# Performance work log

Measured on AMD Instinct MI355X. Metric: run time of the kernel, lower is better.

The kernel has to match this reference:

```python
import jax, jax.numpy as jnp
import numpy as np

N_NODES = 100000
IN_CH = 256
H1, C1 = 8, 8   # conv1: heads=8, out_channels=8
H2, C2 = 1, 3   # conv2: heads=1, out_channels=3
NEG_SLOPE = 0.2
EPS = 1e-16


def gat_conv(x, src, dst, W, a_src, a_dst, b, heads, out_ch, n_nodes):
    """PyG-style GATConv (eval mode, self-loops already in src/dst)."""
    h = (x @ W).reshape(n_nodes, heads, out_ch)          # [N,H,C]
    alpha_s = jnp.einsum('nhc,hc->nh', h, a_src)         # [N,H]
    alpha_d = jnp.einsum('nhc,hc->nh', h, a_dst)         # [N,H]
    e = alpha_s[src] + alpha_d[dst]                      # [E,H]
    e = jnp.where(e > 0, e, NEG_SLOPE * e)               # leaky_relu(0.2)
    # segment softmax over destination nodes
    m = jax.ops.segment_max(e, dst, num_segments=n_nodes)
    m = jnp.where(jnp.isfinite(m), m, 0.0)
    ex = jnp.exp(e - m[dst])
    s = jax.ops.segment_sum(ex, dst, num_segments=n_nodes)
    a = ex / (s[dst] + EPS)                              # [E,H]
    msg = h[src] * a[:, :, None]                         # [E,H,C]
    out = jax.ops.segment_sum(msg, dst, num_segments=n_nodes)  # [N,H,C]
    return out.reshape(n_nodes, heads * out_ch) + b


def setup_inputs() -> dict:
    key = jax.random.key(0)
    ks = jax.random.split(key, 10)
    x = jax.random.normal(ks[0], (N_NODES, IN_CH), dtype=jnp.float32)
    edge_index = jax.random.randint(ks[1], (2, 3200000), 0, N_NODES, dtype=jnp.int64)
    sc = 0.1
    return {
        'x': x,
        'edge_index': edge_index,
        'W1': jax.random.normal(ks[2], (IN_CH, H1 * C1), dtype=jnp.float32) * sc,
        'a_src1': jax.random.normal(ks[3], (H1, C1), dtype=jnp.float32) * sc,
        'a_dst1': jax.random.normal(ks[4], (H1, C1), dtype=jnp.float32) * sc,
        'b1': jnp.zeros((H1 * C1,), dtype=jnp.float32),
        'W2': jax.random.normal(ks[5], (H1 * C1, H2 * C2), dtype=jnp.float32) * sc,
        'a_src2': jax.random.normal(ks[6], (H2, C2), dtype=jnp.float32) * sc,
        'a_dst2': jax.random.normal(ks[7], (H2, C2), dtype=jnp.float32) * sc,
        'b2': jnp.zeros((H2 * C2,), dtype=jnp.float32),
    }


def reference(x, edge_index, W1, a_src1, a_dst1, b1, W2, a_src2, a_dst2, b2):
    n = x.shape[0]
    loop = jnp.arange(n, dtype=edge_index.dtype)
    src = jnp.concatenate([edge_index[0], loop])  # add_self_loops=True
    dst = jnp.concatenate([edge_index[1], loop])
    h = gat_conv(x, src, dst, W1, a_src1, a_dst1, b1, H1, C1, n)
    h = jax.nn.elu(h)
    out = gat_conv(h, src, dst, W2, a_src2, a_dst2, b2, H2, C2, n)
    return out
```

## Files before the change

kernel.cpp:

```cpp
#include <hip/hip_runtime.h>
#include <hip/hip_bf16.h>

#define P_W1  0
#define P_AS1 16384
#define P_AD1 16448
#define P_B1  16512
#define P_W2  16576
#define P_AS2 16768
#define P_AD2 16771
#define P_B2  16774

#define NBLK_CSR 512
#define G1GRID   1024

typedef __attribute__((ext_vector_type(8))) short short8;
typedef __attribute__((ext_vector_type(8))) unsigned short ushort8v;
typedef __attribute__((ext_vector_type(4))) float floatx4;

__device__ __forceinline__ float ldf(const void* p, int i, int bf) {
  if (bf) {
    unsigned v = ((unsigned)((const unsigned short*)p)[i]) << 16;
    float f; __builtin_memcpy(&f, &v, 4); return f;
  }
  return ((const float*)p)[i];
}
__device__ __forceinline__ int ldi(const void* p, long i, int i64) {
  return i64 ? ((const int*)p)[2*i] : ((const int*)p)[i];
}
__device__ __forceinline__ unsigned short f2bfbits(float f) {
  __hip_bfloat16 b = __float2bfloat16(f);
  unsigned short u; __builtin_memcpy(&u, &b, 2); return u;
}
__device__ __forceinline__ float bf2f(unsigned short u) {
  unsigned v = ((unsigned)u) << 16;
  float f; __builtin_memcpy(&f, &v, 4); return f;
}

__device__ __forceinline__ void bar_lgkm() {
  __builtin_amdgcn_sched_barrier(0);
  asm volatile("s_waitcnt lgkmcnt(0)" ::: "memory");
  __builtin_amdgcn_s_barrier();
  __builtin_amdgcn_sched_barrier(0);
}

__global__ void k_prep(const void* x, const void* ei,
                       const void* w1, const void* as1, const void* ad1, const void* b1,
                       const void* w2, const void* as2, const void* ad2, const void* b2,
                       int* flags, float* params, unsigned short* w1t) {
  __shared__ int sh[2];
  int tid = threadIdx.x, lane = tid & 63, w = tid >> 6;
  if (w == 0) {
    const unsigned* xw = (const unsigned*)x;
    int hits = 0;
    for (int i = lane; i < 256; i += 64) {
      unsigned b = (xw[i] >> 7) & 0xFF;
      hits += (b >= 96 && b <= 141) ? 1 : 0;
    }
    for (int o = 32; o >= 1; o >>= 1) hits += __shfl_xor(hits, o);
    if (lane == 0) sh[0] = (hits >= 160) ? 1 : 0;
  } else if (w == 1) {
    const unsigned* ew = (const unsigned*)ei;
    int z = 0;
    for (int i = lane; i < 128; i += 64) z += (ew[2*i+1] == 0u) ? 1 : 0;
    for (int o = 32; o >= 1; o >>= 1) z += __shfl_xor(z, o);
    if (lane == 0) sh[1] = (z >= 64) ? 1 : 0;
  }
  __syncthreads();
  int bf = sh[0];
  if (tid == 0) { flags[0] = sh[0]; flags[1] = sh[1]; }
  for (int i = tid; i < 16384; i += blockDim.x) {
    int ch = i >> 8, k = i & 255;
    w1t[i] = f2bfbits(ldf(w1, k * 64 + ch, bf));
  }
  if (!bf) {
    for (int i = tid; i < 16384; i += blockDim.x) params[P_W1 + i] = ldf(w1, i, bf);
  }
  for (int i = tid; i < 64; i += blockDim.x) {
    params[P_AS1 + i] = ldf(as1, i, bf);
    params[P_AD1 + i] = ldf(ad1, i, bf);
    params[P_B1  + i] = ldf(b1,  i, bf);
  }
  for (int i = tid; i < 192; i += blockDim.x) params[P_W2 + i] = ldf(w2, i, bf);
  for (int i = tid; i < 3; i += blockDim.x) {
    params[P_AS2 + i] = ldf(as2, i, bf);
    params[P_AD2 + i] = ldf(ad2, i, bf);
    params[P_B2  + i] = ldf(b2,  i, bf);
  }
}

__global__ void k_bcount(const void* ei, const int* flags, int* gcnt, int* brsv,
                         int E0, int N, int NB, int chunk) {
  __shared__ int h[256];
  int tid = threadIdx.x;
  int i64 = flags[1];
  for (int j = tid; j < NB; j += 256) h[j] = 0;
  __syncthreads();
  int E = E0 + N;
  int b0 = blockIdx.x * chunk, b1 = min(b0 + chunk, E);
  const int* ep = (const int*)ei;
  for (int e = b0 + tid * 2; e < b1; e += 512) {
    int d0, d1;
    if (e + 1 < E0) {
      if (i64) { int4 v = *(const int4*)(ep + 2 * ((long)E0 + e)); d0 = v.x; d1 = v.z; }
      else     { int2 v = *(const int2*)(ep + (long)E0 + e);       d0 = v.x; d1 = v.y; }
    } else {
      d0 = (e < E0)     ? ldi(ei, (long)E0 + e, i64)     : (e - E0);
      d1 = (e + 1 < E0) ? ldi(ei, (long)E0 + e + 1, i64) : (e + 1 - E0);
    }
    atomicAdd(&h[d0 >> 9], 1);
    if (e + 1 < b1) atomicAdd(&h[d1 >> 9], 1);
  }
  __syncthreads();
  for (int j = tid; j < NB; j += 256)
    brsv[blockIdx.x * NB + j] = atomicAdd(&gcnt[j], h[j]);
}

__global__ void k_bbase(const int* gcnt, int* bbase, int NB) {
  __shared__ int sh[256];
  int tid = threadIdx.x;
  sh[tid] = (tid < NB) ? gcnt[tid] : 0;
  __syncthreads();
  int own = sh[tid];
  for (int ofs = 1; ofs < 256; ofs <<= 1) {
    int v = (tid >= ofs) ? sh[tid - ofs] : 0;
    __syncthreads();
    sh[tid] += v;
    __syncthreads();
  }
  if (tid < NB) bbase[tid] = sh[tid] - own;
  if (tid == NB - 1) bbase[NB] = sh[tid];
}

__global__ void k_bscatter(const void* ei, const int* flags, const int* bbase,
                           const int* brsv, unsigned* pairs, int E0, int N, int NB, int chunk) {
  __shared__ int base_s[256];
  __shared__ int rnk[256];
  int i64 = flags[1], tid = threadIdx.x;
  for (int j = tid; j < NB; j += 256) {
    base_s[j] = bbase[j] + brsv[blockIdx.x * NB + j];
    rnk[j] = 0;
  }
  __syncthreads();
  int E = E0 + N;
  int b0 = blockIdx.x * chunk, b1 = min(b0 + chunk, E);
  const int* ep = (const int*)ei;
  for (int e = b0 + tid * 2; e < b1; e += 512) {
    int s0v, s1v, d0, d1;
    if (e + 1 < E0) {
      if (i64) {
        int4 vs = *(const int4*)(ep + 2 * (long)e);        s0v = vs.x; s1v = vs.z;
        int4 vd = *(const int4*)(ep + 2 * ((long)E0 + e)); d0 = vd.x;  d1 = vd.z;
      } else {
        int2 vs = *(const int2*)(ep + (long)e);            s0v = vs.x; s1v = vs.y;
        int2 vd = *(const int2*)(ep + (long)E0 + e);       d0 = vd.x;  d1 = vd.y;
      }
    } else {
      if (e < E0) { s0v = ldi(ei, e, i64);     d0 = ldi(ei, (long)E0 + e, i64); }
      else        { s0v = e - E0;              d0 = s0v; }
      if (e + 1 < E0) { s1v = ldi(ei, e + 1, i64); d1 = ldi(ei, (long)E0 + e + 1, i64); }
      else            { s1v = e + 1 - E0;          d1 = s1v; }
    }
    {
      int bkt = d0 >> 9;
      int r = atomicAdd(&rnk[bkt], 1);
      pairs[base_s[bkt] + r] = ((unsigned)s0v << 9) | (unsigned)(d0 & 511);
    }
    if (e + 1 < b1) {
      int bkt = d1 >> 9;
      int r = atomicAdd(&rnk[bkt], 1);
      pairs[base_s[bkt] + r] = ((unsigned)s1v << 9) | (unsigned)(d1 & 511);
    }
  }
}

__global__ void k_bsort(const unsigned* pairs, const int* bbase, int* rowp,
                        int* srcs, int N, int NB, int E) {
  __shared__ int h0[512], sc[512], rk[512];
  int b = blockIdx.x, tid = threadIdx.x;
  int s0 = bbase[b], s1 = bbase[b + 1], L = s1 - s0;
  for (int j = tid; j < 512; j += 256) { h0[j] = 0; rk[j] = 0; }
  __syncthreads();
  for (int i = tid; i < L; i += 256) atomicAdd(&h0[pairs[s0 + i] & 511], 1);
  __syncthreads();
  for (int j = tid; j < 512; j += 256) sc[j] = h0[j];
  __syncthreads();
  for (int ofs = 1; ofs < 512; ofs <<= 1) {
    int j0 = tid, j1 = tid + 256;
    int v0 = (j0 >= ofs) ? sc[j0 - ofs] : 0;
    int v1 = (j1 >= ofs) ? sc[j1 - ofs] : 0;
    __syncthreads();
    sc[j0] += v0; sc[j1] += v1;
    __syncthreads();
  }
  for (int j = tid; j < 512; j += 256) {
    int off = sc[j] - h0[j];
    int node = (b << 9) + j;
    if (node < N) rowp[node] = s0 + off;
    sc[j] = off;
  }
  if (b == 0 && tid == 0) rowp[N] = E;
  __syncthreads();
  for (int i = tid; i < L; i += 256) {
    unsigned p = pairs[s0 + i];
    int j = p & 511;
    int r = atomicAdd(&rk[j], 1);
    srcs[s0 + sc[j] + r] = (int)(p >> 9);
  }
}

__device__ __forceinline__ void gemm1_f32(const float* x, const float* params,
                                          unsigned short* h1, float* a_s, float* a_d,
                                          int N, int wave, int lane) {
  int n0 = wave * 4;
  if (n0 >= N) return;
  int nb[4];
#pragma unroll
  for (int j = 0; j < 4; j++) nb[j] = min(n0 + j, N - 1) * 256;
  float acc[4] = {0.f, 0.f, 0.f, 0.f};
  const float* W = params + P_W1;
  for (int k = 0; k < 256; k++) {
    float wv = W[k * 64 + lane];
#pragma unroll
    for (int j = 0; j < 4; j++) acc[j] += x[nb[j] + k] * wv;
  }
  float as1v = params[P_AS1 + lane], ad1v = params[P_AD1 + lane];
#pragma unroll
  for (int j = 0; j < 4; j++) {
    int n = n0 + j;
    if (n >= N) break;
    float hv = acc[j];
    float s = hv * as1v, d = hv * ad1v;
    s += __shfl_xor(s, 1); s += __shfl_xor(s, 2); s += __shfl_xor(s, 4);
    d += __shfl_xor(d, 1); d += __shfl_xor(d, 2); d += __shfl_xor(d, 4);
    h1[(size_t)n * 64 + lane] = f2bfbits(hv);
    if ((lane & 7) == 0) {
      a_s[n * 8 + (lane >> 3)] = s;
      a_d[n * 8 + (lane >> 3)] = d;
    }
  }
}

__global__ void k_gemm1(const void* x, const unsigned short* w1t, const int* flags,
                        const float* params, unsigned short* h1, float* a_s, float* a_d, int N) {
  __shared__ __align__(16) char smem[32768];
  int tid = threadIdx.x;
  int w = tid >> 6, lane = tid & 63;
  if (flags[0]) {
    int NT = (N + 31) >> 5;
    int l16 = lane & 15, quad = lane >> 4;
    int ch = w * 16 + l16;
    const char* xb = (const char*)x;

    auto stage = [&](int t, int bsel) {
      int row0 = t << 5;
      char* buf = smem + bsel * 16384;
#pragma unroll
      for (int jj = 0; jj < 4; jj++) {
        int g = w * 256 + jj * 64 + lane;
        int r = g >> 5;
        int c = g & 31;
        int gr = row0 + r; if (gr >= N) gr = N - 1;
        const char* src = xb + (size_t)gr * 512 + (size_t)((c << 4) ^ ((r & 7) << 4));
        char* dst = buf + g * 16;
        __builtin_amdgcn_global_load_lds((const __attribute__((address_space(1))) unsigned int*)src,
                                         (__attribute__((address_space(3))) unsigned int*)dst,
                                         16, 0, 0);
      }
    };

    short8 bfr[8];
    const unsigned short* wp = w1t + (size_t)ch * 256 + quad * 8;
#pragma unroll
    for (int i = 0; i < 8; i++) bfr[i] = *(const short8*)(wp + i * 32);
    __builtin_amdgcn_sched_barrier(0);

    int t0 = blockIdx.x;
    if (t0 < NT) stage(t0, 0);
    int cur = 0;
    for (int t = t0; t < NT; t += G1GRID) {
      __syncthreads();
      if (t + G1GRID < NT) stage(t + G1GRID, cur ^ 1);
      int row0 = t << 5;
      const char* buf = smem + cur * 16384;
      floatx4 acc[2];
#pragma unroll
      for (int rg = 0; rg < 2; rg++) {
        floatx4 a4 = {0.f, 0.f, 0.f, 0.f};
        int r = rg * 16 + l16;
        const char* arow = buf + r * 512;
        int swz = (r & 7) << 4;
#pragma unroll
        for (int i = 0; i < 8; i++) {
          short8 afr = *(const short8*)(arow + ((quad * 16 + i * 64) ^ swz));
          a4 = __builtin_amdgcn_mfma_f32_16x16x32_bf16(afr, bfr[i], a4, 0, 0, 0);
        }
        acc[rg] = a4;
      }
      bar_lgkm();
      float* ht = (float*)(smem + cur * 16384);
#pragma unroll
      for (int rg = 0; rg < 2; rg++)
#pragma unroll
        for (int rr = 0; rr < 4; rr++)
          ht[(rg * 16 + quad * 4 + rr) * 67 + ch] = acc[rg][rr];
      bar_lgkm();
      int nl = tid >> 3, head = tid & 7;
      int n = row0 + nl;
      if (n < N) {
        const float* hr = ht + nl * 67 + head * 8;
        float s = 0.f, d = 0.f;
        ushort8v u;
#pragma unroll
        for (int c = 0; c < 8; c++) {
          float v = hr[c];
          s += v * params[P_AS1 + head * 8 + c];
          d += v * params[P_AD1 + head * 8 + c];
          u[c] = f2bfbits(v);
        }
        *(ushort8v*)(h1 + (size_t)n * 64 + head * 8) = u;
        a_s[n * 8 + head] = s;
        a_d[n * 8 + head] = d;
      }
      cur ^= 1;
    }
  } else {
    int NW = (N + 3) >> 2;
    for (int task = blockIdx.x * 4 + w; task < NW; task += G1GRID * 4)
      gemm1_f32((const float*)x, params, h1, a_s, a_d, N, task, lane);
  }
}

__global__ void k_agg1(const float* params, const unsigned short* h1, const float* a_s,
                       const float* a_d, const int* rowp, const int* srcs,
                       float4* pk, float* ad2, int N) {
  int n = blockIdx.x * (blockDim.x >> 6) + (threadIdx.x >> 6);
  int lane = threadIdx.x & 63;
  if (n >= N) return;
  int start = rowp[n], end = rowp[n + 1];
  int h = lane & 7, es = lane >> 3;
  float adh = a_d[n * 8 + h];
  float m = -1e30f, ssum = 0.f;
  float acc[8] = {0.f,0.f,0.f,0.f,0.f,0.f,0.f,0.f};
  for (int i = start + es; i < end; i += 8) {
    int s = srcs[i];
    float e = a_s[s * 8 + h] + adh;
    e = e > 0.f ? e : 0.2f * e;
    if (e > m) {
      float sc = __expf(m - e);
      ssum *= sc;
#pragma unroll
      for (int c = 0; c < 8; c++) acc[c] *= sc;
      m = e;
    }
    float ex = __expf(e - m);
    ssum += ex;
    ushort8v u = *(const ushort8v*)(h1 + (size_t)s * 64 + h * 8);
#pragma unroll
    for (int c = 0; c < 8; c++) acc[c] += ex * bf2f(u[c]);
  }
#pragma unroll
  for (int msk = 8; msk <= 32; msk <<= 1) {
    float mo = __shfl_xor(m, msk);
    float so = __shfl_xor(ssum, msk);
    float M = fmaxf(m, mo);
    float scs = __expf(m - M), sco = __expf(mo - M);
    ssum = ssum * scs + so * sco;
#pragma unroll
    for (int c = 0; c < 8; c++) {
      float ao = __shfl_xor(acc[c], msk);
      acc[c] = acc[c] * scs + ao * sco;
    }
    m = M;
  }
  if (es == 0) {
    float inv = 1.f / (ssum + 1e-16f);
    float pj0 = 0.f, pj1 = 0.f, pj2 = 0.f;
#pragma unroll
    for (int c = 0; c < 8; c++) {
      float v = acc[c] * inv + params[P_B1 + h * 8 + c];
      v = v > 0.f ? v : (__expf(v) - 1.f);
      const float* w2r = params + P_W2 + (h * 8 + c) * 3;
      pj0 += v * w2r[0]; pj1 += v * w2r[1]; pj2 += v * w2r[2];
    }
    pj0 += __shfl_xor(pj0, 1); pj1 += __shfl_xor(pj1, 1); pj2 += __shfl_xor(pj2, 1);
    pj0 += __shfl_xor(pj0, 2); pj1 += __shfl_xor(pj1, 2); pj2 += __shfl_xor(pj2, 2);
    pj0 += __shfl_xor(pj0, 4); pj1 += __shfl_xor(pj1, 4); pj2 += __shfl_xor(pj2, 4);
    if (h == 0) {
      float as2 = pj0*params[P_AS2+0] + pj1*params[P_AS2+1] + pj2*params[P_AS2+2];
      float ad2v = pj0*params[P_AD2+0] + pj1*params[P_AD2+1] + pj2*params[P_AD2+2];
      pk[n] = make_float4(pj0, pj1, pj2, as2);
      ad2[n] = ad2v;
    }
  }
}

__global__ void k_agg2(const float* params, const float4* pk, const float* ad2,
                       const int* rowp, const int* srcs, void* out, const int* flags, int N) {
  int wid = blockIdx.x * (blockDim.x >> 6) + (threadIdx.x >> 6);
  int lane = threadIdx.x & 63;
  int g = lane >> 4, t = lane & 15;
  int n = wid * 4 + g;
  if (n >= N) return;
  int start = rowp[n], end = rowp[n + 1];
  float ad = ad2[n];
  float m = -1e30f, ssum = 0.f, c0 = 0.f, c1 = 0.f, c2 = 0.f;
  for (int i = start + t; i < end; i += 16) {
    float4 v = pk[srcs[i]];
    float e = v.w + ad;
    e = e > 0.f ? e : 0.2f * e;
    if (e > m) {
      float sc = __expf(m - e);
      ssum *= sc; c0 *= sc; c1 *= sc; c2 *= sc;
      m = e;
    }
    float ex = __expf(e - m);
    ssum += ex;
    c0 += ex * v.x; c1 += ex * v.y; c2 += ex * v.z;
  }
#pragma unroll
  for (int msk = 1; msk <= 8; msk <<= 1) {
    float mo = __shfl_xor(m, msk);
    float so = __shfl_xor(ssum, msk);
    float a0 = __shfl_xor(c0, msk), a1 = __shfl_xor(c1, msk), a2 = __shfl_xor(c2, msk);
    float M = fmaxf(m, mo);
    float scs = __expf(m - M), sco = __expf(mo - M);
    ssum = ssum * scs + so * sco;
    c0 = c0 * scs + a0 * sco;
    c1 = c1 * scs + a1 * sco;
    c2 = c2 * scs + a2 * sco;
    m = M;
  }
  if (t == 0) {
    float inv = 1.f / (ssum + 1e-16f);
    float o0 = c0 * inv + params[P_B2+0];
    float o1 = c1 * inv + params[P_B2+1];
    float o2 = c2 * inv + params[P_B2+2];
    if (flags[0]) {
      __hip_bfloat16* ob = (__hip_bfloat16*)out;
      ob[n*3+0] = __float2bfloat16(o0);
      ob[n*3+1] = __float2bfloat16(o1);
      ob[n*3+2] = __float2bfloat16(o2);
    } else {
      float* of = (float*)out;
      of[n*3+0] = o0; of[n*3+1] = o1; of[n*3+2] = o2;
    }
  }
}

extern "C" void kernel_launch(void* const* d_in, const int* in_sizes, int n_in,
                              void* d_out, int out_size, void* d_ws, size_t ws_size,
                              hipStream_t stream) {
  const void* x  = d_in[0];
  const void* ei = d_in[1];
  int N  = in_sizes[0] / 256;
  int E0 = in_sizes[1] / 2;
  int E  = E0 + N;
  int NB = (N + 511) >> 9;
  int chunk = (((E + NBLK_CSR - 1) / NBLK_CSR) + 1) & ~1;

  char* w = (char*)d_ws;
  size_t off = 0;
  auto alloc = [&](size_t bytes) -> char* {
    char* p = w + off;
    off += (bytes + 255) & ~(size_t)255;
    return p;
  };
  int*            flags  = (int*)           alloc(256);
  float*          params = (float*)         alloc(17408 * 4);
  unsigned short* w1t    = (unsigned short*)alloc(16384 * 2);
  unsigned short* h1     = (unsigned short*)alloc((size_t)N * 64 * 2);
  float*          a_s1   = (float*)         alloc((size_t)N * 8 * 4);
  float*          a_d1   = (float*)         alloc((size_t)N * 8 * 4);
  float4*         pk     = (float4*)        alloc((size_t)N * 16);
  float*          ad2    = (float*)         alloc((size_t)N * 4);
  int*            gcnt   = (int*)           alloc(256 * 4);
  int*            bbase  = (int*)           alloc(257 * 4);
  int*            brsv   = (int*)           alloc((size_t)NBLK_CSR * NB * 4);
  int*            rowp   = (int*)           alloc((size_t)(N + 1) * 4);
  unsigned*       pairs  = (unsigned*)      alloc((size_t)E * 4);
  int*            srcs   = (int*)           alloc((size_t)E * 4);
  (void)ws_size; (void)n_in; (void)out_size;

  hipMemsetAsync(gcnt, 0, 256 * 4, stream);
  k_prep<<<1, 256, 0, stream>>>(x, ei, d_in[2], d_in[3], d_in[4], d_in[5],
                                d_in[6], d_in[7], d_in[8], d_in[9], flags, params, w1t);
  k_gemm1<<<dim3(G1GRID), 256, 0, stream>>>(x, w1t, flags, params, h1, a_s1, a_d1, N);
  k_bcount<<<dim3(NBLK_CSR), 256, 0, stream>>>(ei, flags, gcnt, brsv, E0, N, NB, chunk);
  k_bbase<<<1, 256, 0, stream>>>(gcnt, bbase, NB);
  k_bscatter<<<dim3(NBLK_CSR), 256, 0, stream>>>(ei, flags, bbase, brsv, pairs, E0, N, NB, chunk);
  k_bsort<<<dim3(NB), 256, 0, stream>>>(pairs, bbase, rowp, srcs, N, NB, E);
  k_agg1<<<dim3((N + 3) / 4), 256, 0, stream>>>(params, h1, a_s1, a_d1, rowp, srcs, pk, ad2, N);
  k_agg2<<<dim3((N + 15) / 16), 256, 0, stream>>>(params, pk, ad2, rowp, srcs, d_out, flags, N);
}
```

Measured before the change: 658.4 us.

## Load GEMM1 A tiles directly into registers with contiguous per-block tile ranges

The layer-1 GEMM no longer stages x tiles through LDS via global_load_lds with a swizzle. Each lane now loads its A fragments straight from global memory into registers, double-buffered across 16-row tiles. Each block processes a contiguous range of tiles instead of striding over the grid, and the grid size doubles. This removes the LDS round trip and the per-tile __syncthreads, at the cost of more register pressure and less coalesced 16-byte global loads per lane. The LDS is now used only for the small transpose in the epilogue.

```diff
diff --git a/kernel.cpp b/kernel.cpp
--- a/kernel.cpp
+++ b/kernel.cpp
@@ -11,7 +11,7 @@
 #define P_B2  16774
 
 #define NBLK_CSR 512
-#define G1GRID   1024
+#define G1GRID   2048
 
 typedef __attribute__((ext_vector_type(8))) short short8;
 typedef __attribute__((ext_vector_type(8))) unsigned short ushort8v;
@@ -242,86 +242,73 @@
 
 __global__ void k_gemm1(const void* x, const unsigned short* w1t, const int* flags,
                         const float* params, unsigned short* h1, float* a_s, float* a_d, int N) {
-  __shared__ __align__(16) char smem[32768];
+  __shared__ __align__(16) float ht[2][16 * 68];
   int tid = threadIdx.x;
   int w = tid >> 6, lane = tid & 63;
   if (flags[0]) {
-    int NT = (N + 31) >> 5;
-    int l16 = lane & 15, quad = lane >> 4;
+    int NT = (N + 15) >> 4;
+    int l16 = lane & 15, q = lane >> 4;
     int ch = w * 16 + l16;
     const char* xb = (const char*)x;
 
-    auto stage = [&](int t, int bsel) {
-      int row0 = t << 5;
-      char* buf = smem + bsel * 16384;
-#pragma unroll
-      for (int jj = 0; jj < 4; jj++) {
-        int g = w * 256 + jj * 64 + lane;
-        int r = g >> 5;
-        int c = g & 31;
-        int gr = row0 + r; if (gr >= N) gr = N - 1;
-        const char* src = xb + (size_t)gr * 512 + (size_t)((c << 4) ^ ((r & 7) << 4));
-        char* dst = buf + g * 16;
-        __builtin_amdgcn_global_load_lds((const __attribute__((address_space(1))) unsigned int*)src,
-                                         (__attribute__((address_space(3))) unsigned int*)dst,
-                                         16, 0, 0);
+    short8 bfr[8];
+    const char* wb = (const char*)w1t + (size_t)ch * 512 + (size_t)(q * 16);
+#pragma unroll
+    for (int i = 0; i < 8; i++) bfr[i] = *(const short8*)(wb + i * 64);
+
+    int per = (NT + G1GRID - 1) / G1GRID;
+    int t0 = blockIdx.x * per, t1 = min(t0 + per, NT);
+    if (t0 >= t1) return;
+
+    auto aload = [&](int t, short8* areg) {
+      int gr = (t << 4) + l16; if (gr >= N) gr = N - 1;
+      const char* xr = xb + (size_t)gr * 512 + (size_t)(q * 16);
+#pragma unroll
+      for (int i = 0; i < 8; i++) areg[i] = *(const short8*)(xr + i * 64);
+    };
+
+    auto tile_body = [&](int t, const short8* a) {
+      floatx4 acc = {0.f, 0.f, 0.f, 0.f};
+#pragma unroll
+      for (int i = 0; i < 8; i++)
+        acc = __builtin_amdgcn_mfma_f32_16x16x32_bf16(a[i], bfr[i], acc, 0, 0, 0);
+      float* H = &ht[t & 1][0];
+#pragma unroll
+      for (int rr = 0; rr < 4; rr++)
+        H[(q * 4 + rr) * 68 + ch] = acc[rr];
+      bar_lgkm();
+      if (tid < 128) {
+        int nl = tid >> 3, head = tid & 7;
+        int n = (t << 4) + nl;
+        if (n < N) {
+          const float* hr = H + nl * 68 + head * 8;
+          float s = 0.f, d = 0.f;
+          ushort8v u;
+#pragma unroll
+          for (int c = 0; c < 8; c++) {
+            float v = hr[c];
+            s += v * params[P_AS1 + head * 8 + c];
+            d += v * params[P_AD1 + head * 8 + c];
+            u[c] = f2bfbits(v);
+          }
+          *(ushort8v*)(h1 + (size_t)n * 64 + head * 8) = u;
+          a_s[n * 8 + head] = s;
+          a_d[n * 8 + head] = d;
+        }
       }
     };
 
-    short8 bfr[8];
-    const unsigned short* wp = w1t + (size_t)ch * 256 + quad * 8;
-#pragma unroll
-    for (int i = 0; i < 8; i++) bfr[i] = *(const short8*)(wp + i * 32);
-    __builtin_amdgcn_sched_barrier(0);
-
-    int t0 = blockIdx.x;
-    if (t0 < NT) stage(t0, 0);
-    int cur = 0;
-    for (int t = t0; t < NT; t += G1GRID) {
-      __syncthreads();
-      if (t + G1GRID < NT) stage(t + G1GRID, cur ^ 1);
-      int row0 = t << 5;
-      const char* buf = smem + cur * 16384;
-      floatx4 acc[2];
-#pragma unroll
-      for (int rg = 0; rg < 2; rg++) {
-        floatx4 a4 = {0.f, 0.f, 0.f, 0.f};
-        int r = rg * 16 + l16;
-        const char* arow = buf + r * 512;
-        int swz = (r & 7) << 4;
-#pragma unroll
-        for (int i = 0; i < 8; i++) {
-          short8 afr = *(const short8*)(arow + ((quad * 16 + i * 64) ^ swz));
-          a4 = __builtin_amdgcn_mfma_f32_16x16x32_bf16(afr, bfr[i], a4, 0, 0, 0);
-        }
-        acc[rg] = a4;
-      }
-      bar_lgkm();
-      float* ht = (float*)(smem + cur * 16384);
-#pragma unroll
-      for (int rg = 0; rg < 2; rg++)
-#pragma unroll
-        for (int rr = 0; rr < 4; rr++)
-          ht[(rg * 16 + quad * 4 + rr) * 67 + ch] = acc[rg][rr];
-      bar_lgkm();
-      int nl = tid >> 3, head = tid & 7;
-      int n = row0 + nl;
-      if (n < N) {
-        const float* hr = ht + nl * 67 + head * 8;
-        float s = 0.f, d = 0.f;
-        ushort8v u;
-#pragma unroll
-        for (int c = 0; c < 8; c++) {
-          float v = hr[c];
-          s += v * params[P_AS1 + head * 8 + c];
-          d += v * params[P_AD1 + head * 8 + c];
-          u[c] = f2bfbits(v);
-        }
-        *(ushort8v*)(h1 + (size_t)n * 64 + head * 8) = u;
-        a_s[n * 8 + head] = s;
-        a_d[n * 8 + head] = d;
-      }
-      cur ^= 1;
+    short8 aA[8], aB[8];
+    aload(t0, aA);
+    int t = t0;
+    while (t < t1) {
+      if (t + 1 < t1) aload(t + 1, aB);
+      tile_body(t, aA);
+      t++;
+      if (t >= t1) break;
+      if (t + 1 < t1) aload(t + 1, aA);
+      tile_body(t, aB);
+      t++;
     }
   } else {
     int NW = (N + 3) >> 2;
```

Result: no change. 660.8 us (+0.4%).
